# Kernel tuning notes

Measured on AMD Instinct MI355X. Metric: run time of the kernel, lower is better.

Reference implementation:

```python
import jax, jax.numpy as jnp
import numpy as np

NUM_GROUPS = 17
NUM_OCCLUDED = 10
TEMP = 0.1


def setup_inputs() -> dict:
    key = jax.random.key(0)
    k1, k2 = jax.random.split(key)
    B, N, D = 128, 577, 768
    x = jax.random.normal(k1, (B, N, D), dtype=jnp.float32)
    # xavier_uniform-like scale for (D, G) weight
    bound = float(np.sqrt(6.0 / (D + NUM_GROUPS)))
    group_weights = jax.random.uniform(k2, (D, NUM_GROUPS), dtype=jnp.float32, minval=-bound, maxval=bound)
    return {"x": x, "group_weights": group_weights}


def _l2_normalize(v):
    # matches F.normalize(dim=-1, eps=1e-12)
    return v / jnp.maximum(jnp.linalg.norm(v, axis=-1, keepdims=True), 1e-12)


def reference(x, group_weights):
    B, N, D = x.shape
    cls_token = x[:, 0, :]            # (B, D)
    patch_tokens = x[:, 1:, :]        # (B, P, D), P = N-1

    # cosine similarity of each patch with cls token
    sim = jnp.einsum('bpd,bd->bp', _l2_normalize(patch_tokens), _l2_normalize(cls_token))  # (B, P)

    # k least-similar patches are "occluded" -> zero them out
    _, occ_idx = jax.lax.top_k(-sim, NUM_OCCLUDED)  # (B, K)
    mask = jnp.ones_like(sim).at[jnp.arange(B)[:, None], occ_idx].set(0.0)  # (B, P)
    non_occ = patch_tokens * mask[..., None]  # (B, P, D)

    # attention-style group pooling; softmax over groups (dim=1)
    scores = jnp.einsum('dg,bpd->bgp', group_weights, non_occ) / TEMP  # (B, G, P)
    attn = jax.nn.softmax(scores, axis=1)
    group_features = jnp.einsum('bgp,bpd->bgd', attn, non_occ)  # (B, G, D)

    # pack [global_feat, group_feat_1..G] as (B, 1+G, D)
    feats = jnp.concatenate([cls_token[:, None, :], group_features], axis=1)
    return feats, attn
```

## Files before the change

kernel.cpp:

```cpp
#include <hip/hip_runtime.h>
#include <math.h>

#define B_ 128
#define NTOK 577
#define P_ 576
#define D_ 768
#define G_ 17
#define KOCC 10
#define INV_TEMP 10.0f
#define U17 (1.0f / 17.0f)
#define NPART 9

#define OFF_WT 0
#define OFF_SIM (G_ * D_)
#define OFF_OCC (OFF_SIM + B_ * P_)
#define OFF_GFP (OFF_OCC + B_ * KOCC)
#define GFP_SLAB ((size_t)B_ * G_ * D_)

__global__ __launch_bounds__(256) void k0_wt(const float* __restrict__ gw,
                                             float* __restrict__ wt) {
    int g = blockIdx.x;
    for (int d = threadIdx.x; d < D_; d += 256)
        wt[g * D_ + d] = gw[d * G_ + g];
}

__global__ __launch_bounds__(256) void k0_zero(float* __restrict__ feats) {
    int b = blockIdx.x;
    float4 z = {0.f, 0.f, 0.f, 0.f};
    float4* fb = (float4*)(feats + (size_t)b * 18 * D_ + D_);
    for (int i = threadIdx.x; i < G_ * D_ / 4; i += 256) fb[i] = z;
}

__global__ __launch_bounds__(256) void k13_fused(const float* __restrict__ x,
                                                 const float* __restrict__ wt,
                                                 float* __restrict__ sim,
                                                 float* __restrict__ attn,
                                                 float* __restrict__ gfp,
                                                 float* __restrict__ feats) {
    __shared__ __align__(16) float buf[2][18 * 64];
    __shared__ __align__(16) float atile[19 * 68];
    int tid = threadIdx.x;
    int b = blockIdx.y, chunk = blockIdx.x;
    const float* clsrow = x + (size_t)b * NTOK * D_;

    for (int i = tid; i < 288; i += 256) {
        int r = i >> 4, c = i & 15;
        const float* src = (r < 17) ? (wt + r * D_ + c * 4) : (clsrow + c * 4);
        *(float4*)&buf[0][r * 64 + c * 4] = *(const float4*)src;
    }
    int lane = tid & 63, wave = tid >> 6;
    int lr = lane & 15, row4 = lane >> 4;
    int pbase = wave * 16 + row4 * 4;
    const float* xp0 = x + ((size_t)(b * NTOK + 1 + chunk * 64 + pbase)) * D_ + lr * 4;

    float4 xv[4], xn[4];
    #pragma unroll
    for (int m = 0; m < 4; ++m) xv[m] = *(const float4*)(xp0 + (size_t)m * D_);

    float s[19][4];
    #pragma unroll
    for (int i = 0; i < 19; ++i)
        #pragma unroll
        for (int m = 0; m < 4; ++m) s[i][m] = 0.f;
    __syncthreads();

    for (int kc = 0; kc < 12; ++kc) {
        int cb = kc & 1, nb = cb ^ 1;
        if (kc < 11) {
            #pragma unroll
            for (int m = 0; m < 4; ++m)
                xn[m] = *(const float4*)(xp0 + (kc + 1) * 64 + (size_t)m * D_);
            for (int i = tid; i < 288; i += 256) {
                int r = i >> 4, c = i & 15;
                const float* src = (r < 17) ? (wt + r * D_ + (kc + 1) * 64 + c * 4)
                                            : (clsrow + (kc + 1) * 64 + c * 4);
                *(float4*)&buf[nb][r * 64 + c * 4] = *(const float4*)src;
            }
        }
        #pragma unroll
        for (int g = 0; g < 18; ++g) {
            float4 w4 = *(const float4*)&buf[cb][g * 64 + lr * 4];
            #pragma unroll
            for (int m = 0; m < 4; ++m)
                s[g][m] = fmaf(xv[m].x, w4.x, fmaf(xv[m].y, w4.y,
                          fmaf(xv[m].z, w4.z, fmaf(xv[m].w, w4.w, s[g][m]))));
        }
        #pragma unroll
        for (int m = 0; m < 4; ++m)
            s[18][m] = fmaf(xv[m].x, xv[m].x, fmaf(xv[m].y, xv[m].y,
                       fmaf(xv[m].z, xv[m].z, fmaf(xv[m].w, xv[m].w, s[18][m]))));
        #pragma unroll
        for (int m = 0; m < 4; ++m) xv[m] = xn[m];
        __syncthreads();
    }

    #pragma unroll
    for (int off = 8; off >= 1; off >>= 1)
        #pragma unroll
        for (int i = 0; i < 19; ++i)
            #pragma unroll
            for (int m = 0; m < 4; ++m)
                s[i][m] += __shfl_xor(s[i][m], off, 16);

    #pragma unroll
    for (int g = 0; g < 19; ++g) {
        if (lr == ((g < 16) ? g : 15)) {
            float4 v = {s[g][0], s[g][1], s[g][2], s[g][3]};
            *(float4*)&atile[g * 68 + pbase] = v;
        }
    }
    __syncthreads();

    if (tid < 64) {
        int p = chunk * 64 + tid;
        float v[17];
        float mx = -3.0e38f;
        #pragma unroll
        for (int g = 0; g < 17; ++g) {
            v[g] = atile[g * 68 + tid];
            mx = fmaxf(mx, v[g]);
        }
        float tot = 0.f;
        #pragma unroll
        for (int g = 0; g < 17; ++g) {
            v[g] = __expf((v[g] - mx) * INV_TEMP);
            tot += v[g];
        }
        float inv = 1.0f / tot;
        float* ap = attn + ((size_t)b * G_) * P_ + p;
        #pragma unroll
        for (int g = 0; g < 17; ++g) {
            float a = v[g] * inv;
            ap[(size_t)g * P_] = a;
            atile[g * 68 + tid] = a;
        }
        float cd = atile[17 * 68 + tid];
        float sq = atile[18 * 68 + tid];
        sim[(size_t)b * P_ + p] = cd / fmaxf(sqrtf(sq), 1e-12f);
    }
    __syncthreads();

    if (tid < 192) {
        const float* xb = x + ((size_t)(b * NTOK + 1 + chunk * 64)) * D_ + tid * 4;
        float4 acc[G_];
        #pragma unroll
        for (int g = 0; g < G_; ++g) acc[g] = make_float4(0.f, 0.f, 0.f, 0.f);

        float4 c0 = *(const float4*)(xb + (size_t)0 * D_);
        float4 c1 = *(const float4*)(xb + (size_t)1 * D_);
        float4 c2 = *(const float4*)(xb + (size_t)2 * D_);
        float4 c3 = *(const float4*)(xb + (size_t)3 * D_);
        for (int pp = 0; pp < 64; pp += 4) {
            float4 n0, n1, n2, n3;
            if (pp + 4 < 64) {
                n0 = *(const float4*)(xb + (size_t)(pp + 4) * D_);
                n1 = *(const float4*)(xb + (size_t)(pp + 5) * D_);
                n2 = *(const float4*)(xb + (size_t)(pp + 6) * D_);
                n3 = *(const float4*)(xb + (size_t)(pp + 7) * D_);
            }
            #pragma unroll
            for (int g = 0; g < G_; ++g) {
                float4 a = *(const float4*)&atile[g * 68 + pp];
                acc[g].x = fmaf(a.x, c0.x, fmaf(a.y, c1.x, fmaf(a.z, c2.x, fmaf(a.w, c3.x, acc[g].x))));
                acc[g].y = fmaf(a.x, c0.y, fmaf(a.y, c1.y, fmaf(a.z, c2.y, fmaf(a.w, c3.y, acc[g].y))));
                acc[g].z = fmaf(a.x, c0.z, fmaf(a.y, c1.z, fmaf(a.z, c2.z, fmaf(a.w, c3.z, acc[g].z))));
                acc[g].w = fmaf(a.x, c0.w, fmaf(a.y, c1.w, fmaf(a.z, c2.w, fmaf(a.w, c3.w, acc[g].w))));
            }
            c0 = n0; c1 = n1; c2 = n2; c3 = n3;
        }
        if (gfp) {
            float* gb = gfp + ((size_t)(chunk * B_ + b) * G_) * D_ + tid * 4;
            #pragma unroll
            for (int g = 0; g < G_; ++g) *(float4*)(gb + (size_t)g * D_) = acc[g];
        } else {
            float* fb = feats + ((size_t)(b * 18) + 1) * D_ + tid * 4;
            #pragma unroll
            for (int g = 0; g < G_; ++g) {
                atomicAdd(fb + (size_t)g * D_ + 0, acc[g].x);
                atomicAdd(fb + (size_t)g * D_ + 1, acc[g].y);
                atomicAdd(fb + (size_t)g * D_ + 2, acc[g].z);
                atomicAdd(fb + (size_t)g * D_ + 3, acc[g].w);
            }
        }
    }
}

__global__ __launch_bounds__(64) void k2_occl(const float* __restrict__ sim,
                                              int* __restrict__ occ_idx) {
    int b = blockIdx.x, lane = threadIdx.x;
    int base = lane * 9;
    float v[9];
    #pragma unroll
    for (int j = 0; j < 9; ++j) v[j] = sim[(size_t)b * P_ + base + j];
    for (int t = 0; t < KOCC; ++t) {
        float mv = 3.0e38f;
        int mi = 1 << 30;
        #pragma unroll
        for (int j = 0; j < 9; ++j) {
            if (v[j] < mv) { mv = v[j]; mi = base + j; }
        }
        #pragma unroll
        for (int off = 1; off < 64; off <<= 1) {
            float ov = __shfl_xor(mv, off, 64);
            int oi = __shfl_xor(mi, off, 64);
            if (ov < mv || (ov == mv && oi < mi)) { mv = ov; mi = oi; }
        }
        if (lane == 0) occ_idx[b * KOCC + t] = mi;
        int loc = mi - base;
        if (loc >= 0 && loc < 9) v[loc] = 3.0e38f;
    }
}

__global__ __launch_bounds__(192) void k4_fin(const float* __restrict__ x,
                                              const int* __restrict__ occ_idx,
                                              const float* __restrict__ gfp,
                                              float* __restrict__ attn,
                                              float* __restrict__ feats,
                                              int nparts) {
    __shared__ float ao[G_ * KOCC];
    __shared__ int op[KOCC];
    int b = blockIdx.x, tid = threadIdx.x;
    if (tid < KOCC) op[tid] = occ_idx[b * KOCC + tid];
    __syncthreads();
    if (tid < G_ * KOCC) {
        int g = tid / KOCC, t = tid - g * KOCC;
        float* ap = attn + ((size_t)b * G_ + g) * P_ + op[t];
        ao[tid] = *ap;
        *ap = U17;
    }
    __syncthreads();

    float* fb = feats + (size_t)b * 18 * D_ + tid * 4;
    *(float4*)fb = *(const float4*)(x + (size_t)b * NTOK * D_ + tid * 4);

    float4 acc[G_];
    if (nparts == 0) {
        #pragma unroll
        for (int g = 0; g < G_; ++g)
            acc[g] = *(const float4*)(fb + (size_t)(1 + g) * D_);
    } else {
        #pragma unroll
        for (int g = 0; g < G_; ++g) acc[g] = make_float4(0.f, 0.f, 0.f, 0.f);
        for (int pc = 0; pc < nparts; ++pc) {
            const float* gb = gfp + ((size_t)(pc * B_ + b) * G_) * D_ + tid * 4;
            #pragma unroll
            for (int g = 0; g < G_; ++g) {
                float4 v = *(const float4*)(gb + (size_t)g * D_);
                acc[g].x += v.x; acc[g].y += v.y; acc[g].z += v.z; acc[g].w += v.w;
            }
        }
    }
    for (int t = 0; t < KOCC; ++t) {
        float4 xo = *(const float4*)(x + ((size_t)(b * NTOK) + 1 + op[t]) * D_ + tid * 4);
        #pragma unroll
        for (int g = 0; g < G_; ++g) {
            float a = ao[g * KOCC + t];
            acc[g].x = fmaf(-a, xo.x, acc[g].x);
            acc[g].y = fmaf(-a, xo.y, acc[g].y);
            acc[g].z = fmaf(-a, xo.z, acc[g].z);
            acc[g].w = fmaf(-a, xo.w, acc[g].w);
        }
    }
    #pragma unroll
    for (int g = 0; g < G_; ++g)
        *(float4*)(fb + (size_t)(1 + g) * D_) = acc[g];
}

extern "C" void kernel_launch(void* const* d_in, const int* in_sizes, int n_in,
                              void* d_out, int out_size, void* d_ws, size_t ws_size,
                              hipStream_t stream) {
    const float* x  = (const float*)d_in[0];
    const float* gw = (const float*)d_in[1];
    float* feats = (float*)d_out;
    float* attn  = (float*)d_out + (size_t)B_ * 18 * D_;
    float* wt      = (float*)d_ws + OFF_WT;
    float* sim     = (float*)d_ws + OFF_SIM;
    int*   occ_idx = (int*)((float*)d_ws + OFF_OCC);
    float* gfp     = (float*)d_ws + OFF_GFP;

    bool use_gfp = (OFF_GFP + (size_t)NPART * GFP_SLAB) * 4 <= ws_size;

    k0_wt<<<G_, 256, 0, stream>>>(gw, wt);
    if (!use_gfp) k0_zero<<<B_, 256, 0, stream>>>(feats);
    k13_fused<<<dim3(NPART, B_), 256, 0, stream>>>(x, wt, sim, attn,
                                                   use_gfp ? gfp : nullptr, feats);
    k2_occl<<<B_, 64, 0, stream>>>(sim, occ_idx);
    k4_fin<<<B_, 192, 0, stream>>>(x, occ_idx, gfp, attn, feats,
                                   use_gfp ? NPART : 0);
}
```

Before: 420.4 us.

## Split fused score/pool kernel into separate scoring and pooling passes

The fused kernel becomes two kernels. k1_score computes the scores, softmax and similarity, and now stages the whole weight matrix plus the cls row in shared memory once, which removes the per-chunk double buffering and its barriers. A new k3_part kernel does the attention-weighted pooling over 96-patch chunks, split into 6 parts, reading attn back from global memory. The split costs a second full read of x (about 227 MB) plus an extra launch, in exchange for less synchronisation and fewer partial slabs. The large shared-memory weight tile (about 55 KB) may also lower occupancy.

```diff
diff --git a/kernel.cpp b/kernel.cpp
--- a/kernel.cpp
+++ b/kernel.cpp
@@ -9,7 +9,8 @@
 #define KOCC 10
 #define INV_TEMP 10.0f
 #define U17 (1.0f / 17.0f)
-#define NPART 9
+#define NPART 6
+#define PC_ 96
 
 #define OFF_WT 0
 #define OFF_SIM (G_ * D_)
@@ -31,67 +32,62 @@
     for (int i = threadIdx.x; i < G_ * D_ / 4; i += 256) fb[i] = z;
 }
 
-__global__ __launch_bounds__(256) void k13_fused(const float* __restrict__ x,
-                                                 const float* __restrict__ wt,
-                                                 float* __restrict__ sim,
-                                                 float* __restrict__ attn,
-                                                 float* __restrict__ gfp,
-                                                 float* __restrict__ feats) {
-    __shared__ __align__(16) float buf[2][18 * 64];
+__global__ __launch_bounds__(256) void k1_score(const float* __restrict__ x,
+                                                const float* __restrict__ wt,
+                                                float* __restrict__ sim,
+                                                float* __restrict__ attn) {
+    __shared__ __align__(16) float wl[18 * 768];
     __shared__ __align__(16) float atile[19 * 68];
     int tid = threadIdx.x;
     int b = blockIdx.y, chunk = blockIdx.x;
     const float* clsrow = x + (size_t)b * NTOK * D_;
 
-    for (int i = tid; i < 288; i += 256) {
-        int r = i >> 4, c = i & 15;
+    for (int i = tid; i < 18 * 192; i += 256) {
+        int r = i / 192, c = i - r * 192;
         const float* src = (r < 17) ? (wt + r * D_ + c * 4) : (clsrow + c * 4);
-        *(float4*)&buf[0][r * 64 + c * 4] = *(const float4*)src;
-    }
+        *(float4*)&wl[r * 768 + c * 4] = *(const float4*)src;
+    }
+
     int lane = tid & 63, wave = tid >> 6;
     int lr = lane & 15, row4 = lane >> 4;
     int pbase = wave * 16 + row4 * 4;
     const float* xp0 = x + ((size_t)(b * NTOK + 1 + chunk * 64 + pbase)) * D_ + lr * 4;
 
-    float4 xv[4], xn[4];
-    #pragma unroll
-    for (int m = 0; m < 4; ++m) xv[m] = *(const float4*)(xp0 + (size_t)m * D_);
+    float4 x0[4], x1[4], x2[4];
+    #pragma unroll
+    for (int m = 0; m < 4; ++m) x0[m] = *(const float4*)(xp0 + (size_t)m * D_);
+    #pragma unroll
+    for (int m = 0; m < 4; ++m) x1[m] = *(const float4*)(xp0 + 64 + (size_t)m * D_);
 
     float s[19][4];
     #pragma unroll
     for (int i = 0; i < 19; ++i)
         #pragma unroll
         for (int m = 0; m < 4; ++m) s[i][m] = 0.f;
-    __syncthreads();
-
+
+    __syncthreads();
+
+    #pragma unroll
     for (int kc = 0; kc < 12; ++kc) {
-        int cb = kc & 1, nb = cb ^ 1;
-        if (kc < 11) {
+        if (kc < 10) {
             #pragma unroll
             for (int m = 0; m < 4; ++m)
-                xn[m] = *(const float4*)(xp0 + (kc + 1) * 64 + (size_t)m * D_);
-            for (int i = tid; i < 288; i += 256) {
-                int r = i >> 4, c = i & 15;
-                const float* src = (r < 17) ? (wt + r * D_ + (kc + 1) * 64 + c * 4)
-                                            : (clsrow + (kc + 1) * 64 + c * 4);
-                *(float4*)&buf[nb][r * 64 + c * 4] = *(const float4*)src;
-            }
+                x2[m] = *(const float4*)(xp0 + (kc + 2) * 64 + (size_t)m * D_);
         }
         #pragma unroll
         for (int g = 0; g < 18; ++g) {
-            float4 w4 = *(const float4*)&buf[cb][g * 64 + lr * 4];
+            float4 w4 = *(const float4*)&wl[g * 768 + kc * 64 + lr * 4];
             #pragma unroll
             for (int m = 0; m < 4; ++m)
-                s[g][m] = fmaf(xv[m].x, w4.x, fmaf(xv[m].y, w4.y,
-                          fmaf(xv[m].z, w4.z, fmaf(xv[m].w, w4.w, s[g][m]))));
+                s[g][m] = fmaf(x0[m].x, w4.x, fmaf(x0[m].y, w4.y,
+                          fmaf(x0[m].z, w4.z, fmaf(x0[m].w, w4.w, s[g][m]))));
         }
         #pragma unroll
         for (int m = 0; m < 4; ++m)
-            s[18][m] = fmaf(xv[m].x, xv[m].x, fmaf(xv[m].y, xv[m].y,
-                       fmaf(xv[m].z, xv[m].z, fmaf(xv[m].w, xv[m].w, s[18][m]))));
-        #pragma unroll
-        for (int m = 0; m < 4; ++m) xv[m] = xn[m];
-        __syncthreads();
+            s[18][m] = fmaf(x0[m].x, x0[m].x, fmaf(x0[m].y, x0[m].y,
+                       fmaf(x0[m].z, x0[m].z, fmaf(x0[m].w, x0[m].w, s[18][m]))));
+        #pragma unroll
+        for (int m = 0; m < 4; ++m) { x0[m] = x1[m]; x1[m] = x2[m]; }
     }
 
     #pragma unroll
@@ -129,59 +125,10 @@
         float inv = 1.0f / tot;
         float* ap = attn + ((size_t)b * G_) * P_ + p;
         #pragma unroll
-        for (int g = 0; g < 17; ++g) {
-            float a = v[g] * inv;
-            ap[(size_t)g * P_] = a;
-            atile[g * 68 + tid] = a;
-        }
+        for (int g = 0; g < 17; ++g) ap[(size_t)g * P_] = v[g] * inv;
         float cd = atile[17 * 68 + tid];
         float sq = atile[18 * 68 + tid];
         sim[(size_t)b * P_ + p] = cd / fmaxf(sqrtf(sq), 1e-12f);
-    }
-    __syncthreads();
-
-    if (tid < 192) {
-        const float* xb = x + ((size_t)(b * NTOK + 1 + chunk * 64)) * D_ + tid * 4;
-        float4 acc[G_];
-        #pragma unroll
-        for (int g = 0; g < G_; ++g) acc[g] = make_float4(0.f, 0.f, 0.f, 0.f);
-
-        float4 c0 = *(const float4*)(xb + (size_t)0 * D_);
-        float4 c1 = *(const float4*)(xb + (size_t)1 * D_);
-        float4 c2 = *(const float4*)(xb + (size_t)2 * D_);
-        float4 c3 = *(const float4*)(xb + (size_t)3 * D_);
-        for (int pp = 0; pp < 64; pp += 4) {
-            float4 n0, n1, n2, n3;
-            if (pp + 4 < 64) {
-                n0 = *(const float4*)(xb + (size_t)(pp + 4) * D_);
-                n1 = *(const float4*)(xb + (size_t)(pp + 5) * D_);
-                n2 = *(const float4*)(xb + (size_t)(pp + 6) * D_);
-                n3 = *(const float4*)(xb + (size_t)(pp + 7) * D_);
-            }
-            #pragma unroll
-            for (int g = 0; g < G_; ++g) {
-                float4 a = *(const float4*)&atile[g * 68 + pp];
-                acc[g].x = fmaf(a.x, c0.x, fmaf(a.y, c1.x, fmaf(a.z, c2.x, fmaf(a.w, c3.x, acc[g].x))));
-                acc[g].y = fmaf(a.x, c0.y, fmaf(a.y, c1.y, fmaf(a.z, c2.y, fmaf(a.w, c3.y, acc[g].y))));
-                acc[g].z = fmaf(a.x, c0.z, fmaf(a.y, c1.z, fmaf(a.z, c2.z, fmaf(a.w, c3.z, acc[g].z))));
-                acc[g].w = fmaf(a.x, c0.w, fmaf(a.y, c1.w, fmaf(a.z, c2.w, fmaf(a.w, c3.w, acc[g].w))));
-            }
-            c0 = n0; c1 = n1; c2 = n2; c3 = n3;
-        }
-        if (gfp) {
-            float* gb = gfp + ((size_t)(chunk * B_ + b) * G_) * D_ + tid * 4;
-            #pragma unroll
-            for (int g = 0; g < G_; ++g) *(float4*)(gb + (size_t)g * D_) = acc[g];
-        } else {
-            float* fb = feats + ((size_t)(b * 18) + 1) * D_ + tid * 4;
-            #pragma unroll
-            for (int g = 0; g < G_; ++g) {
-                atomicAdd(fb + (size_t)g * D_ + 0, acc[g].x);
-                atomicAdd(fb + (size_t)g * D_ + 1, acc[g].y);
-                atomicAdd(fb + (size_t)g * D_ + 2, acc[g].z);
-                atomicAdd(fb + (size_t)g * D_ + 3, acc[g].w);
-            }
-        }
     }
 }
 
@@ -208,6 +155,67 @@
         if (lane == 0) occ_idx[b * KOCC + t] = mi;
         int loc = mi - base;
         if (loc >= 0 && loc < 9) v[loc] = 3.0e38f;
+    }
+}
+
+__global__ __launch_bounds__(192) void k3_part(const float* __restrict__ x,
+                                               const float* __restrict__ attn,
+                                               float* __restrict__ gfp,
+                                               float* __restrict__ feats) {
+    __shared__ __align__(16) float am[G_ * PC_];
+    int tid = threadIdx.x;
+    int pc = blockIdx.x, b = blockIdx.y;
+    int p0 = pc * PC_;
+
+    for (int i = tid; i < G_ * PC_; i += 192) {
+        int g = i / PC_;
+        int pp = i - g * PC_;
+        am[i] = attn[((size_t)b * G_ + g) * P_ + p0 + pp];
+    }
+    __syncthreads();
+
+    const float* xb = x + ((size_t)(b * NTOK) + 1 + p0) * D_ + tid * 4;
+    float4 acc[G_];
+    #pragma unroll
+    for (int g = 0; g < G_; ++g) acc[g] = make_float4(0.f, 0.f, 0.f, 0.f);
+
+    float4 c0 = *(const float4*)(xb + (size_t)0 * D_);
+    float4 c1 = *(const float4*)(xb + (size_t)1 * D_);
+    float4 c2 = *(const float4*)(xb + (size_t)2 * D_);
+    float4 c3 = *(const float4*)(xb + (size_t)3 * D_);
+
+    for (int pp = 0; pp < PC_; pp += 4) {
+        float4 n0, n1, n2, n3;
+        if (pp + 4 < PC_) {
+            n0 = *(const float4*)(xb + (size_t)(pp + 4) * D_);
+            n1 = *(const float4*)(xb + (size_t)(pp + 5) * D_);
+            n2 = *(const float4*)(xb + (size_t)(pp + 6) * D_);
+            n3 = *(const float4*)(xb + (size_t)(pp + 7) * D_);
+        }
+        #pragma unroll
+        for (int g = 0; g < G_; ++g) {
+            float4 a = *(const float4*)&am[g * PC_ + pp];
+            acc[g].x = fmaf(a.x, c0.x, fmaf(a.y, c1.x, fmaf(a.z, c2.x, fmaf(a.w, c3.x, acc[g].x))));
+            acc[g].y = fmaf(a.x, c0.y, fmaf(a.y, c1.y, fmaf(a.z, c2.y, fmaf(a.w, c3.y, acc[g].y))));
+            acc[g].z = fmaf(a.x, c0.z, fmaf(a.y, c1.z, fmaf(a.z, c2.z, fmaf(a.w, c3.z, acc[g].z))));
+            acc[g].w = fmaf(a.x, c0.w, fmaf(a.y, c1.w, fmaf(a.z, c2.w, fmaf(a.w, c3.w, acc[g].w))));
+        }
+        c0 = n0; c1 = n1; c2 = n2; c3 = n3;
+    }
+
+    if (gfp) {
+        float* gb = gfp + ((size_t)(pc * B_ + b) * G_) * D_ + tid * 4;
+        #pragma unroll
+        for (int g = 0; g < G_; ++g) *(float4*)(gb + (size_t)g * D_) = acc[g];
+    } else {
+        float* fb = feats + ((size_t)(b * 18) + 1) * D_ + tid * 4;
+        #pragma unroll
+        for (int g = 0; g < G_; ++g) {
+            atomicAdd(fb + (size_t)g * D_ + 0, acc[g].x);
+            atomicAdd(fb + (size_t)g * D_ + 1, acc[g].y);
+            atomicAdd(fb + (size_t)g * D_ + 2, acc[g].z);
+            atomicAdd(fb + (size_t)g * D_ + 3, acc[g].w);
+        }
     }
 }
 
@@ -282,9 +290,9 @@
 
     k0_wt<<<G_, 256, 0, stream>>>(gw, wt);
     if (!use_gfp) k0_zero<<<B_, 256, 0, stream>>>(feats);
-    k13_fused<<<dim3(NPART, B_), 256, 0, stream>>>(x, wt, sim, attn,
-                                                   use_gfp ? gfp : nullptr, feats);
+    k1_score<<<dim3(9, B_), 256, 0, stream>>>(x, wt, sim, attn);
     k2_occl<<<B_, 64, 0, stream>>>(sim, occ_idx);
+    k3_part<<<dim3(NPART, B_), 192, 0, stream>>>(x, attn, use_gfp ? gfp : nullptr, feats);
     k4_fin<<<B_, 192, 0, stream>>>(x, occ_idx, gfp, attn, feats,
                                    use_gfp ? NPART : 0);
 }
```

Result: slower. 435.6 us (+3.6%).
